# Kernel tuning notes

Measured on AMD Instinct MI355X. Metric: run time of the kernel, lower is better.

## Reference

```python
import jax, jax.numpy as jnp
import numpy as np

B, S, D = 2, 2048, 512
H, HD = 8, 64  # num_heads, hidden_dim; H*HD == D
FF = 2048
EPS = 1e-5


def layer_norm(x, gamma, beta):
    mu = jnp.mean(x, axis=-1, keepdims=True)
    var = jnp.mean(jnp.square(x - mu), axis=-1, keepdims=True)
    return (x - mu) * jax.lax.rsqrt(var + EPS) * gamma + beta


def setup_inputs() -> dict:
    key = jax.random.key(0)
    ks = jax.random.split(key, 16)
    s = 0.02
    return {
        "Q": jax.random.normal(ks[0], (B, S, D), jnp.float32),
        "K": jax.random.normal(ks[1], (B, S, D), jnp.float32),
        "V": jax.random.normal(ks[2], (B, S, D), jnp.float32),
        "mask": jax.random.randint(ks[3], (B, S, S), 0, 2, jnp.int32),
        "Wq": jax.random.normal(ks[4], (D, H * HD), jnp.float32) * s,
        "Wk": jax.random.normal(ks[5], (D, H * HD), jnp.float32) * s,
        "Wv": jax.random.normal(ks[6], (D, H * HD), jnp.float32) * s,
        "Wo": jax.random.normal(ks[7], (H * HD, D), jnp.float32) * s,
        "bo": jnp.zeros((D,), jnp.float32),
        "gamma": jnp.ones((D,), jnp.float32),
        "beta": jnp.zeros((D,), jnp.float32),
        "W1": jax.random.normal(ks[8], (D, FF), jnp.float32) * s,
        "b1": jnp.zeros((FF,), jnp.float32),
        "W2": jax.random.normal(ks[9], (FF, D), jnp.float32) * s,
        "b2": jnp.zeros((D,), jnp.float32),
    }


def reference(Q, K, V, mask, Wq, Wk, Wv, Wo, bo, gamma, beta, W1, b1, W2, b2):
    # NOTE: original torch code calls Z.masked_fill(...) non-inplace and drops
    # the result, so `mask` has no effect on the math. Sequence=False.
    X = V
    # Faithful (interleaving) reshape: [B, S, H*HD] -> [B*H, S, HD]
    q = (Q @ Wq).reshape(B * H, -1, HD)
    k = (K @ Wk).reshape(B * H, -1, HD)
    v = (V @ Wv).reshape(B * H, -1, HD)
    scale = jnp.sqrt(jnp.float32(D))  # sqrt(input_size[2]), not sqrt(hidden_dim)
    scores = jnp.einsum('bqd,bkd->bqk', q, k) / scale  # [B*H, S, S]
    attn = jax.nn.softmax(scores, axis=2)
    Z = jnp.einsum('bqk,bkd->bqd', attn, v)            # [B*H, S, HD]
    Z = Z.reshape(B, -1, H * HD) @ Wo + bo             # [B, S, D]
    Z = layer_norm(X + Z, gamma, beta)
    ffn = (Z @ W1 + b1) @ W2 + b2                      # no activation in source
    return layer_norm(Z + ffn, gamma, beta)
```

## Files before the change

kernel.cpp:

```cpp
#include <hip/hip_runtime.h>
#include <hip/hip_bf16.h>


typedef __hip_bfloat16 bf16;
typedef short s16x8 __attribute__((ext_vector_type(8)));
typedef short s16x4 __attribute__((ext_vector_type(4)));
typedef float f32x4 __attribute__((ext_vector_type(4)));

#if __has_builtin(__builtin_amdgcn_exp2f)
#define EXP2F(x) __builtin_amdgcn_exp2f(x)
#else
#define EXP2F(x) exp2f(x)
#endif

__device__ __forceinline__ int dtypeF32(const void* gamma) {
    return *(const unsigned int*)gamma == 0x3F800000u;
}
__device__ __forceinline__ float inElem(const void* p, size_t i, int f32) {
    return f32 ? ((const float*)p)[i]
               : __bfloat162float(((const bf16*)p)[i]);
}
__device__ __forceinline__ void outElem(void* p, size_t i, float v, int f32) {
    if (f32) ((float*)p)[i] = v;
    else     ((bf16*)p)[i] = __float2bfloat16(v);
}
__device__ __forceinline__ s16x8 load8bf(const void* p, size_t i, int f32) {
    if (f32) {
        const float* s = (const float*)p + i;
        const float4 a = *(const float4*)s;
        const float4 b = *(const float4*)(s + 4);
        bf16 t[8] = {__float2bfloat16(a.x), __float2bfloat16(a.y),
                     __float2bfloat16(a.z), __float2bfloat16(a.w),
                     __float2bfloat16(b.x), __float2bfloat16(b.y),
                     __float2bfloat16(b.z), __float2bfloat16(b.w)};
        return *(const s16x8*)t;
    }
    return *(const s16x8*)((const bf16*)p + i);
}
__device__ __forceinline__ void load8f(const void* p, size_t i, int f32, float* o) {
    if (f32) {
        const float* s = (const float*)p + i;
        const float4 a = *(const float4*)s;
        const float4 b = *(const float4*)(s + 4);
        o[0] = a.x; o[1] = a.y; o[2] = a.z; o[3] = a.w;
        o[4] = b.x; o[5] = b.y; o[6] = b.z; o[7] = b.w;
    } else {
        const s16x8 v = *(const s16x8*)((const bf16*)p + i);
#pragma unroll
        for (int j = 0; j < 8; ++j) o[j] = __bfloat162float(((const bf16*)&v)[j]);
    }
}
__device__ __forceinline__ void store8(void* p, size_t i, const float* v, int f32) {
    if (f32) {
        float4 a = {v[0], v[1], v[2], v[3]};
        float4 b = {v[4], v[5], v[6], v[7]};
        *(float4*)((float*)p + i) = a;
        *(float4*)((float*)p + i + 4) = b;
    } else {
        bf16 t[8];
#pragma unroll
        for (int j = 0; j < 8; ++j) t[j] = __float2bfloat16(v[j]);
        *(s16x8*)((bf16*)p + i) = *(const s16x8*)t;
    }
}

__device__ __forceinline__ void gll16(const bf16* g, unsigned short* l) {
    __builtin_amdgcn_global_load_lds(
        (const __attribute__((address_space(1))) unsigned int*)(const void*)g,
        (__attribute__((address_space(3))) unsigned int*)(void*)l,
        16, 0, 0);
}

__device__ __forceinline__ size_t kfAddr(int row, int col) {
    const int g = row >> 8;
    const int j = ((row & 255) << 3) + (col >> 6);
    const int d = col & 63;
    return ((size_t)g << 17) + ((j >> 4) << 10) + ((d >> 5) << 9) +
           (((d & 31) >> 3) << 7) + ((j & 15) << 3) + (d & 7);
}
__device__ __forceinline__ size_t vfAddr(int row, int col) {
    const int g = row >> 8;
    const int j = ((row & 255) << 3) + (col >> 6);
    const int d = col & 63;
    return ((size_t)g << 17) + ((j >> 4) << 10) + ((d >> 4) << 8) +
           (((j >> 2) & 3) << 6) + ((d & 15) << 2) + (j & 3);
}

__global__ __launch_bounds__(256) void tr_kernel(const void* __restrict__ s0,
                                                 const void* __restrict__ s1,
                                                 const void* __restrict__ s2,
                                                 const void* __restrict__ s3,
                                                 const void* __restrict__ s4,
                                                 bf16* __restrict__ WT4,
                                                 bf16* __restrict__ W2T,
                                                 float scale0,
                                                 const void* __restrict__ gamma,
                                                 const void* __restrict__ bo,
                                                 float* __restrict__ bo_f) {
    const int z = blockIdx.z;
    if (z == 0 && blockIdx.y == 16 && blockIdx.x == 0) {
        const int f32 = dtypeF32(gamma);
        bo_f[threadIdx.x] = inElem(bo, threadIdx.x, f32);
        bo_f[threadIdx.x + 256] = inElem(bo, threadIdx.x + 256, f32);
        return;
    }
    if (z < 4 && blockIdx.y >= 16) return;
    const int f32 = dtypeF32(gamma);
    const void* src = z == 0 ? s0 : (z == 1 ? s1 : (z == 2 ? s2 : (z == 3 ? s3 : s4)));
    const int R = (z == 4) ? 2048 : 512;
    const int C = 512;
    bf16* d = (z == 4) ? W2T : WT4 + (size_t)z * 512 * 512;
    const float sc = (z == 0) ? scale0 : 1.f;
    __shared__ bf16 T[32][33];
    const int tx = threadIdx.x & 31, ty = threadIdx.x >> 5;
    const int c0 = blockIdx.x * 32, r0 = blockIdx.y * 32;
#pragma unroll
    for (int i = 0; i < 4; ++i)
        T[ty + 8 * i][tx] = __float2bfloat16(
            sc * inElem(src, (size_t)(r0 + ty + 8 * i) * C + c0 + tx, f32));
    __syncthreads();
#pragma unroll
    for (int i = 0; i < 4; ++i)
        d[(size_t)(c0 + ty + 8 * i) * R + r0 + tx] = T[tx][ty + 8 * i];
}

__global__ __launch_bounds__(256) void proj_kernel(
    const void* __restrict__ Q, const void* __restrict__ K,
    const void* __restrict__ V, const bf16* __restrict__ WT4,
    bf16* __restrict__ Qp, bf16* __restrict__ KFo, bf16* __restrict__ VFo,
    const bf16* __restrict__ W2T, const void* __restrict__ W1,
    float* __restrict__ Wc32, const void* __restrict__ gamma) {
    __shared__ __align__(16) unsigned short smem[20480];

    const int f32 = dtypeF32(gamma);
    const int tid = threadIdx.x;
    const int w = tid >> 6, lane = tid & 63, quad = lane >> 4, l16 = lane & 15;
    const int sr = tid >> 2, sc = (tid & 3) * 8;
    const int blk = blockIdx.x;

    if (blk < 384) {
        typedef unsigned short AsT[64][32];
        typedef unsigned short BsT[256][32];
        AsT* As = (AsT*)smem;
        BsT* Bs = (BsT*)(smem + 4096);

        const int z = blk >> 7, rem = blk & 127, by = rem >> 1, bx = rem & 1;
        const void* A = z == 0 ? Q : (z == 1 ? K : V);
        const bf16* Bt = WT4 + (size_t)z * 512 * 512;
        const int row0 = by * 64, col0 = bx * 256;

        f32x4 acc[4][4];
#pragma unroll
        for (int rb = 0; rb < 4; ++rb)
#pragma unroll
            for (int nb = 0; nb < 4; ++nb) acc[rb][nb] = (f32x4){0.f, 0.f, 0.f, 0.f};

        const size_t aBase = (size_t)(row0 + sr) * 512 + sc;
        const bf16* gB = Bt + (size_t)(col0 + sr) * 512 + sc;

        {
            const s16x8 a0 = load8bf(A, aBase, f32);
#pragma unroll
            for (int c = 0; c < 4; ++c)
                gll16(gB + (size_t)c * 64 * 512, &Bs[0][c * 64 + sr][sc]);
            *(s16x8*)&As[0][sr][sc] = a0;
        }
        __syncthreads();

        for (int t = 0; t < 16; ++t) {
            const int cur = t & 1, nxt = cur ^ 1;
            s16x8 aN;
            if (t < 15) {
                const int k = (t + 1) * 32;
                aN = load8bf(A, aBase + k, f32);
#pragma unroll
                for (int c = 0; c < 4; ++c)
                    gll16(gB + k + (size_t)c * 64 * 512, &Bs[nxt][c * 64 + sr][sc]);
            }

            s16x8 af[4];
#pragma unroll
            for (int rb = 0; rb < 4; ++rb)
                af[rb] = *(const s16x8*)&As[cur][rb * 16 + l16][quad * 8];
#pragma unroll
            for (int nb = 0; nb < 4; ++nb) {
                const s16x8 bf = *(const s16x8*)&Bs[cur][w * 64 + nb * 16 + l16][quad * 8];
#pragma unroll
                for (int rb = 0; rb < 4; ++rb)
                    acc[rb][nb] = __builtin_amdgcn_mfma_f32_16x16x32_bf16(
                        af[rb], bf, acc[rb][nb], 0, 0, 0);
            }

            if (t < 15) {
                *(s16x8*)&As[nxt][sr][sc] = aN;
                __syncthreads();
            }
        }

#pragma unroll
        for (int rb = 0; rb < 4; ++rb)
#pragma unroll
            for (int nb = 0; nb < 4; ++nb) {
                const int col = col0 + w * 64 + nb * 16 + l16;
#pragma unroll
                for (int r = 0; r < 4; ++r) {
                    const int row = row0 + rb * 16 + quad * 4 + r;
                    const bf16 v = __float2bfloat16(acc[rb][nb][r]);
                    if (z == 0)      Qp[(size_t)row * 512 + col] = v;
                    else if (z == 1) KFo[kfAddr(row, col)] = v;
                    else             VFo[vfAddr(row, col)] = v;
                }
            }
    } else {
        unsigned short (*As)[40] = (unsigned short (*)[40])smem;
        unsigned short (*Bs)[40] = (unsigned short (*)[40])(smem + 2560);

        const int idx = blk - 384;
        const int bx = idx & 3, by = (idx >> 2) & 7, bz = idx >> 5;
        const int N = 512, Kd = 2048, kSlice = 512;
        const int wr = w >> 1, wc = w & 1;
        const int row0 = by * 64, col0 = bx * 128;
        const int kOff = bz * kSlice;
        float* C = Wc32 + (size_t)bz * N * N;

        f32x4 acc[2][4];
#pragma unroll
        for (int rb = 0; rb < 2; ++rb)
#pragma unroll
            for (int nb = 0; nb < 4; ++nb) acc[rb][nb] = (f32x4){0.f, 0.f, 0.f, 0.f};

        for (int k0 = kOff; k0 < kOff + kSlice; k0 += 32) {
            __syncthreads();
            *(s16x8*)&As[sr][sc] = *(const s16x8*)(W2T + (size_t)(row0 + sr) * Kd + k0 + sc);
            *(s16x8*)&Bs[sr][sc] = load8bf(W1, (size_t)(col0 + sr) * Kd + k0 + sc, f32);
            *(s16x8*)&Bs[sr + 64][sc] = load8bf(W1, (size_t)(col0 + sr + 64) * Kd + k0 + sc, f32);
            __syncthreads();

            s16x8 aF[2], bFr[4];
#pragma unroll
            for (int rb = 0; rb < 2; ++rb)
                aF[rb] = *(const s16x8*)&As[wr * 32 + rb * 16 + l16][quad * 8];
#pragma unroll
            for (int nb = 0; nb < 4; ++nb)
                bFr[nb] = *(const s16x8*)&Bs[wc * 64 + nb * 16 + l16][quad * 8];
#pragma unroll
            for (int rb = 0; rb < 2; ++rb)
#pragma unroll
                for (int nb = 0; nb < 4; ++nb)
                    acc[rb][nb] = __builtin_amdgcn_mfma_f32_16x16x32_bf16(
                        aF[rb], bFr[nb], acc[rb][nb], 0, 0, 0);
        }

#pragma unroll
        for (int rb = 0; rb < 2; ++rb)
#pragma unroll
            for (int nb = 0; nb < 4; ++nb) {
                const int col = col0 + wc * 64 + nb * 16 + l16;
#pragma unroll
                for (int r = 0; r < 4; ++r) {
                    const int row = row0 + wr * 32 + rb * 16 + quad * 4 + r;
                    C[(size_t)row * N + col] = acc[rb][nb][r];
                }
            }
    }
}

__global__ __launch_bounds__(512) void attn_mfma_kernel(const bf16* __restrict__ Qp,
                                                        const bf16* __restrict__ KF,
                                                        const bf16* __restrict__ VF,
                                                        bf16* __restrict__ Z) {
    __shared__ __align__(16) unsigned short KsF[2][2][8192];
    __shared__ __align__(16) unsigned short VsF[2][2][8192];

    const int tid = threadIdx.x;
    const int w = tid >> 6;
    const int lane = tid & 63;
    const int quad = lane >> 4;
    const int l16 = lane & 15;
    const int hg = w >> 2;
    const int wl = w & 3;
    const int sg = tid >> 8;
    const int stid = tid & 255;

    const int g = blockIdx.x & 15;
    const int qt = blockIdx.x >> 4;
    const int qbase = g * 2048 + qt * 128 + wl * 32 + l16;

    s16x8 bQ[2][2];
#pragma unroll
    for (int qf = 0; qf < 2; ++qf)
#pragma unroll
        for (int ks = 0; ks < 2; ++ks)
            bQ[qf][ks] = *(const s16x8*)(Qp + (size_t)(qbase + qf * 16) * 64 + ks * 32 + quad * 8);

    f32x4 o[2][4];
    f32x4 oSum[2];
#pragma unroll
    for (int qf = 0; qf < 2; ++qf) {
        oSum[qf] = (f32x4){0.f, 0.f, 0.f, 0.f};
#pragma unroll
        for (int db = 0; db < 4; ++db) o[qf][db] = (f32x4){0.f, 0.f, 0.f, 0.f};
    }
    const s16x4 aOnes = {(short)0x3F80, (short)0x3F80, (short)0x3F80, (short)0x3F80};

    const bf16* KFg = KF + (size_t)g * 131072;
    const bf16* VFg = VF + (size_t)g * 131072;
    const int tb = sg * 8;

#pragma unroll
    for (int c = 0; c < 4; ++c) {
        const int idx = c * 256 + stid;
        gll16(KFg + (size_t)tb * 8192 + idx * 8, &KsF[sg][0][idx * 8]);
        gll16(VFg + (size_t)tb * 8192 + idx * 8, &VsF[sg][0][idx * 8]);
    }
    __syncthreads();

    for (int t = 0; t < 8; ++t) {
        const int cur = t & 1, nxt = cur ^ 1;
        if (t < 7) {
            const bf16* kt = KFg + (size_t)(tb + t + 1) * 8192;
            const bf16* vt = VFg + (size_t)(tb + t + 1) * 8192;
#pragma unroll
            for (int c = 0; c < 4; ++c) {
                const int idx = c * 256 + stid;
                gll16(kt + (size_t)idx * 8, &KsF[sg][nxt][idx * 8]);
                gll16(vt + (size_t)idx * 8, &VsF[sg][nxt][idx * 8]);
            }
        }

#pragma unroll
        for (int h = 0; h < 2; ++h) {
            const unsigned short* Kh = &KsF[hg][cur][h * 4096];
            const unsigned short* Vh = &VsF[hg][cur][h * 4096];

            f32x4 st[2][4];
#pragma unroll
            for (int qf = 0; qf < 2; ++qf)
#pragma unroll
                for (int kb = 0; kb < 4; ++kb) st[qf][kb] = (f32x4){0.f, 0.f, 0.f, 0.f};
#pragma unroll
            for (int kb = 0; kb < 4; ++kb)
#pragma unroll
                for (int ks = 0; ks < 2; ++ks) {
                    const s16x8 aK = *(const s16x8*)&Kh[((kb * 2 + ks) * 64 + lane) * 8];
                    st[0][kb] = __builtin_amdgcn_mfma_f32_16x16x32_bf16(aK, bQ[0][ks], st[0][kb], 0, 0, 0);
                    st[1][kb] = __builtin_amdgcn_mfma_f32_16x16x32_bf16(aK, bQ[1][ks], st[1][kb], 0, 0, 0);
                }

            s16x4 bP[2][4];
#pragma unroll
            for (int qf = 0; qf < 2; ++qf)
#pragma unroll
                for (int kb = 0; kb < 4; ++kb) {
                    const float p0 = EXP2F(st[qf][kb][0]);
                    const float p1 = EXP2F(st[qf][kb][1]);
                    const float p2 = EXP2F(st[qf][kb][2]);
                    const float p3 = EXP2F(st[qf][kb][3]);
                    const unsigned lo = __builtin_amdgcn_perm(
                        __builtin_bit_cast(unsigned, p1), __builtin_bit_cast(unsigned, p0), 0x07060302u);
                    const unsigned hi = __builtin_amdgcn_perm(
                        __builtin_bit_cast(unsigned, p3), __builtin_bit_cast(unsigned, p2), 0x07060302u);
                    union { unsigned u[2]; s16x4 v; } cvt;
                    cvt.u[0] = lo; cvt.u[1] = hi;
                    bP[qf][kb] = cvt.v;
                }

#pragma unroll
            for (int kb = 0; kb < 4; ++kb) {
                oSum[0] = __builtin_amdgcn_mfma_f32_16x16x16bf16_1k(aOnes, bP[0][kb], oSum[0], 0, 0, 0);
                oSum[1] = __builtin_amdgcn_mfma_f32_16x16x16bf16_1k(aOnes, bP[1][kb], oSum[1], 0, 0, 0);
#pragma unroll
                for (int db = 0; db < 4; ++db) {
                    const s16x4 aV = *(const s16x4*)&Vh[((kb * 4 + db) * 64 + lane) * 4];
                    o[0][db] = __builtin_amdgcn_mfma_f32_16x16x16bf16_1k(aV, bP[0][kb], o[0][db], 0, 0, 0);
                    o[1][db] = __builtin_amdgcn_mfma_f32_16x16x16bf16_1k(aV, bP[1][kb], o[1][db], 0, 0, 0);
                }
            }
        }

        if (t < 7) __syncthreads();
    }

    float* mrg = (float*)&KsF[0][0][0];
    __syncthreads();
    if (hg == 1) {
#pragma unroll
        for (int qf = 0; qf < 2; ++qf) {
#pragma unroll
            for (int db = 0; db < 4; ++db)
#pragma unroll
                for (int r = 0; r < 4; ++r)
                    mrg[((qf * 16 + db * 4 + r) << 8) + wl * 64 + lane] = o[qf][db][r];
            mrg[((32 + qf) << 8) + wl * 64 + lane] = oSum[qf][0];
        }
    }
    __syncthreads();
    if (hg == 0) {
#pragma unroll
        for (int qf = 0; qf < 2; ++qf) {
            const float sTot = oSum[qf][0] + mrg[((32 + qf) << 8) + wl * 64 + lane];
            const float inv = 1.f / sTot;
            const size_t qrow = (size_t)(qbase + qf * 16);
#pragma unroll
            for (int db = 0; db < 4; ++db) {
                bf16 tmp[4];
#pragma unroll
                for (int r = 0; r < 4; ++r) {
                    const float vv = o[qf][db][r] +
                        mrg[((qf * 16 + db * 4 + r) << 8) + wl * 64 + lane];
                    tmp[r] = __float2bfloat16(vv * inv);
                }
                *(s16x4*)(Z + qrow * 64 + db * 16 + quad * 4) = *(const s16x4*)tmp;
            }
        }
    }
}

__global__ __launch_bounds__(256) void gemm_bt_kernel(
    const bf16* __restrict__ A, const bf16* __restrict__ Bt,
    const float* __restrict__ bias, bf16* __restrict__ C,
    int N, int K,
    const float* __restrict__ Cf, bf16* __restrict__ WcTo,
    const bf16* __restrict__ W2Tp, const void* __restrict__ b1,
    const void* __restrict__ b2, float* __restrict__ bcO,
    const void* __restrict__ gamma) {
    __shared__ __align__(16) unsigned short As[2][64][32];
    __shared__ __align__(16) unsigned short Bs[2][128][32];

    const int tid = threadIdx.x;
    if (blockIdx.x >= 4) {
        if (blockIdx.x < 8) {
            const int i = (((blockIdx.x - 4) * 64 + blockIdx.y) * 256 + tid) * 4;
            const int MN = 512 * 512;
            const float4 a = *(const float4*)(Cf + i);
            const float4 b4 = *(const float4*)(Cf + i + MN);
            const float4 c = *(const float4*)(Cf + i + 2 * MN);
            const float4 d = *(const float4*)(Cf + i + 3 * MN);
            bf16 t[4] = {__float2bfloat16(a.x + b4.x + c.x + d.x),
                         __float2bfloat16(a.y + b4.y + c.y + d.y),
                         __float2bfloat16(a.z + b4.z + c.z + d.z),
                         __float2bfloat16(a.w + b4.w + c.w + d.w)};
            *(s16x4*)(WcTo + i) = *(const s16x4*)t;
        } else {
            const int f32 = dtypeF32(gamma);
            const int w4 = tid >> 6, lane = tid & 63;
#pragma unroll
            for (int t = 0; t < 2; ++t) {
                const int n = blockIdx.y * 8 + w4 * 2 + t;
                const bf16* rowp = W2Tp + (size_t)n * 2048;
                float s = 0.f;
#pragma unroll
                for (int i = 0; i < 4; ++i) {
                    const int f = lane * 8 + 512 * i;
                    float b1v[8];
                    load8f(b1, f, f32, b1v);
                    const s16x8 r = *(const s16x8*)(rowp + f);
#pragma unroll
                    for (int j = 0; j < 8; ++j)
                        s += b1v[j] * __bfloat162float(((const bf16*)&r)[j]);
                }
#pragma unroll
                for (int off = 32; off; off >>= 1) s += __shfl_xor(s, off);
                if (lane == 0) bcO[n] = s + inElem(b2, n, f32);
            }
        }
        return;
    }

    const int w = tid >> 6, lane = tid & 63, quad = lane >> 4, l16 = lane & 15;
    const int wr = w >> 1, wc = w & 1;
    const int row0 = blockIdx.y * 64, col0 = blockIdx.x * 128;
    const int sr = tid >> 2, sc = (tid & 3) * 8;

    const bf16* gA  = A  + (size_t)(row0 + sr) * K + sc;
    const bf16* gB0 = Bt + (size_t)(col0 + sr) * K + sc;
    const bf16* gB1 = Bt + (size_t)(col0 + sr + 64) * K + sc;

    f32x4 acc[2][4];
#pragma unroll
    for (int rb = 0; rb < 2; ++rb)
#pragma unroll
        for (int nb = 0; nb < 4; ++nb) acc[rb][nb] = (f32x4){0.f, 0.f, 0.f, 0.f};

    const int nst = K >> 5;
    gll16(gA,  &As[0][sr][sc]);
    gll16(gB0, &Bs[0][sr][sc]);
    gll16(gB1, &Bs[0][sr + 64][sc]);
    __syncthreads();

    for (int t = 0; t < nst; ++t) {
        const int cur = t & 1, nxt = cur ^ 1;
        if (t + 1 < nst) {
            const int k = (t + 1) * 32;
            gll16(gA + k,  &As[nxt][sr][sc]);
            gll16(gB0 + k, &Bs[nxt][sr][sc]);
            gll16(gB1 + k, &Bs[nxt][sr + 64][sc]);
        }

        s16x8 aF[2], bF[4];
#pragma unroll
        for (int rb = 0; rb < 2; ++rb)
            aF[rb] = *(const s16x8*)&As[cur][wr * 32 + rb * 16 + l16][quad * 8];
#pragma unroll
        for (int nb = 0; nb < 4; ++nb)
            bF[nb] = *(const s16x8*)&Bs[cur][wc * 64 + nb * 16 + l16][quad * 8];
#pragma unroll
        for (int rb = 0; rb < 2; ++rb)
#pragma unroll
            for (int nb = 0; nb < 4; ++nb)
                acc[rb][nb] = __builtin_amdgcn_mfma_f32_16x16x32_bf16(
                    aF[rb], bF[nb], acc[rb][nb], 0, 0, 0);

        if (t + 1 < nst) __syncthreads();
    }

#pragma unroll
    for (int rb = 0; rb < 2; ++rb)
#pragma unroll
        for (int nb = 0; nb < 4; ++nb) {
            const int col = col0 + wc * 64 + nb * 16 + l16;
            const float bv = bias[col];
#pragma unroll
            for (int r = 0; r < 4; ++r) {
                const int row = row0 + wr * 32 + rb * 16 + quad * 4 + r;
                C[(size_t)row * N + col] = __float2bfloat16(acc[rb][nb][r] + bv);
            }
        }
}

__global__ __launch_bounds__(256) void ln_res_kernel(const void* __restrict__ X, int xMode,
                                                     const bf16* __restrict__ Zin,
                                                     const void* __restrict__ gamma,
                                                     const void* __restrict__ beta,
                                                     void* __restrict__ out, int oMode) {
    const int f = dtypeF32(gamma);
    const int xF = xMode == 2 ? f : xMode;
    const int oF = oMode == 2 ? f : oMode;
    const int row = blockIdx.x * 4 + (threadIdx.x >> 6);
    const int lane = threadIdx.x & 63;
    const size_t rb = (size_t)row * 512;
    const int c0 = lane * 8;

    float v[8];
    load8f(X, rb + c0, xF, v);
    const s16x8 z = *(const s16x8*)(Zin + rb + c0);
    float sum = 0.f, sumsq = 0.f;
#pragma unroll
    for (int i = 0; i < 8; ++i) {
        v[i] += __bfloat162float(((const bf16*)&z)[i]);
        sum += v[i];
        sumsq += v[i] * v[i];
    }
#pragma unroll
    for (int off = 32; off; off >>= 1) {
        sum += __shfl_xor(sum, off);
        sumsq += __shfl_xor(sumsq, off);
    }
    const float mu = sum * (1.f / 512.f);
    const float var = sumsq * (1.f / 512.f) - mu * mu;
    const float rs = rsqrtf(var + 1e-5f);
    float g[8], bt[8], o[8];
    load8f(gamma, c0, f, g);
    load8f(beta, c0, f, bt);
#pragma unroll
    for (int i = 0; i < 8; ++i) o[i] = (v[i] - mu) * rs * g[i] + bt[i];
    store8(out, rb + c0, o, oF);
}

extern "C" void kernel_launch(void* const* d_in, const int* in_sizes, int n_in,
                              void* d_out, int out_size, void* d_ws, size_t ws_size,
                              hipStream_t stream) {
    const void* Q     = d_in[0];
    const void* K     = d_in[1];
    const void* V     = d_in[2];
    const void* Wq    = d_in[4];
    const void* Wk    = d_in[5];
    const void* Wv    = d_in[6];
    const void* Wo    = d_in[7];
    const void* bo    = d_in[8];
    const void* gamma = d_in[9];
    const void* beta  = d_in[10];
    const void* W1    = d_in[11];
    const void* b1    = d_in[12];
    const void* W2    = d_in[13];
    const void* b2    = d_in[14];

    const size_t NT  = (size_t)4096 * 512;
    const size_t WSQ = 512 * 512;
    const size_t W1N = 512 * 2048;

    const size_t NEED = 26000000;
    char* scratch = (ws_size >= NEED) ? (char*)d_ws : (char*)d_in[3];

    bf16* base = (bf16*)scratch;
    bf16* Qp  = base;
    bf16* KF  = Qp + NT;
    bf16* VF  = KF + NT;
    bf16* Zt  = VF + NT;
    bf16* WT4 = Zt + NT;
    bf16* W2T = WT4 + 4 * WSQ;
    bf16* WcT = W2T + W1N;
    float* Wc32 = (float*)(WcT + WSQ);
    float* bc   = Wc32 + 4 * WSQ;
    float* bo_f = bc + 512;
    bf16* Zo = VF;
    bf16* Z1 = KF;
    bf16* Fo = (bf16*)Wc32;

    const dim3 blk(256);
    const float qscale = 1.4426950408889634f * 0.044194173824159216f;

    tr_kernel<<<dim3(16, 64, 5), blk, 0, stream>>>(Wq, Wk, Wv, Wo, W2,
                                                   WT4, W2T, qscale, gamma, bo, bo_f);

    proj_kernel<<<dim3(512), blk, 0, stream>>>(Q, K, V, WT4, Qp, KF, VF,
                                               W2T, W1, Wc32, gamma);

    attn_mfma_kernel<<<dim3(256), dim3(512), 0, stream>>>(Qp, KF, VF, Zt);

    gemm_bt_kernel<<<dim3(9, 64), blk, 0, stream>>>(Zt, WT4 + 3 * WSQ, bo_f, Zo,
                                                    512, 512,
                                                    Wc32, WcT, W2T, b1, b2, bc, gamma);

    ln_res_kernel<<<dim3(1024), blk, 0, stream>>>(V, 2, Zo, gamma, beta, Z1, 0);

    gemm_bt_kernel<<<dim3(4, 64), blk, 0, stream>>>(Z1, WcT, bc, Fo,
                                                    512, 512,
                                                    nullptr, nullptr, nullptr,
                                                    nullptr, nullptr, nullptr, gamma);

    ln_res_kernel<<<dim3(1024), blk, 0, stream>>>(Z1, 0, Fo, gamma, beta, d_out, 2);
}
```

Measured before the change: 199.6 us.

## Double K-tile depth in projection GEMMs and stage epilogue through LDS for vector stores

The QKV projection and the bias GEMM now load 64-wide K tiles per stage instead of 32, which halves the number of barriers and pipeline iterations. The projection epilogue now writes accumulators into a padded, XOR-swizzled LDS tile and then emits 16-byte vector stores into the Q, K-fragment and V-fragment layouts, replacing scattered 2-byte stores computed through kfAddr/vfAddr. In exchange, LDS use per block roughly doubles, which may lower occupancy, and the layout index math becomes more intricate.

```diff
diff --git a/kernel.cpp b/kernel.cpp
--- a/kernel.cpp
+++ b/kernel.cpp
@@ -69,21 +69,6 @@
         (const __attribute__((address_space(1))) unsigned int*)(const void*)g,
         (__attribute__((address_space(3))) unsigned int*)(void*)l,
         16, 0, 0);
-}
-
-__device__ __forceinline__ size_t kfAddr(int row, int col) {
-    const int g = row >> 8;
-    const int j = ((row & 255) << 3) + (col >> 6);
-    const int d = col & 63;
-    return ((size_t)g << 17) + ((j >> 4) << 10) + ((d >> 5) << 9) +
-           (((d & 31) >> 3) << 7) + ((j & 15) << 3) + (d & 7);
-}
-__device__ __forceinline__ size_t vfAddr(int row, int col) {
-    const int g = row >> 8;
-    const int j = ((row & 255) << 3) + (col >> 6);
-    const int d = col & 63;
-    return ((size_t)g << 17) + ((j >> 4) << 10) + ((d >> 4) << 8) +
-           (((j >> 2) & 3) << 6) + ((d & 15) << 2) + (j & 3);
 }
 
 __global__ __launch_bounds__(256) void tr_kernel(const void* __restrict__ s0,
@@ -130,7 +115,7 @@
     bf16* __restrict__ Qp, bf16* __restrict__ KFo, bf16* __restrict__ VFo,
     const bf16* __restrict__ W2T, const void* __restrict__ W1,
     float* __restrict__ Wc32, const void* __restrict__ gamma) {
-    __shared__ __align__(16) unsigned short smem[20480];
+    __shared__ __align__(16) unsigned short smem[40960];
 
     const int f32 = dtypeF32(gamma);
     const int tid = threadIdx.x;
@@ -139,10 +124,8 @@
     const int blk = blockIdx.x;
 
     if (blk < 384) {
-        typedef unsigned short AsT[64][32];
-        typedef unsigned short BsT[256][32];
-        AsT* As = (AsT*)smem;
-        BsT* Bs = (BsT*)(smem + 4096);
+        unsigned short* AsF = smem;
+        unsigned short* BsF = smem + 8192;
 
         const int z = blk >> 7, rem = blk & 127, by = rem >> 1, bx = rem & 1;
         const void* A = z == 0 ? Q : (z == 1 ? K : V);
@@ -156,61 +139,121 @@
             for (int nb = 0; nb < 4; ++nb) acc[rb][nb] = (f32x4){0.f, 0.f, 0.f, 0.f};
 
         const size_t aBase = (size_t)(row0 + sr) * 512 + sc;
-        const bf16* gB = Bt + (size_t)(col0 + sr) * 512 + sc;
 
         {
             const s16x8 a0 = load8bf(A, aBase, f32);
-#pragma unroll
-            for (int c = 0; c < 4; ++c)
-                gll16(gB + (size_t)c * 64 * 512, &Bs[0][c * 64 + sr][sc]);
-            *(s16x8*)&As[0][sr][sc] = a0;
+            const s16x8 a1 = load8bf(A, aBase + 32, f32);
+#pragma unroll
+            for (int c = 0; c < 8; ++c) {
+                const int ch = c * 256 + tid;
+                gll16(Bt + (size_t)(col0 + (ch >> 3)) * 512 + (ch & 7) * 8,
+                      BsF + ch * 8);
+            }
+            *(s16x8*)(AsF + sr * 64 + sc) = a0;
+            *(s16x8*)(AsF + sr * 64 + sc + 32) = a1;
         }
         __syncthreads();
 
-        for (int t = 0; t < 16; ++t) {
+        for (int t = 0; t < 8; ++t) {
             const int cur = t & 1, nxt = cur ^ 1;
-            s16x8 aN;
-            if (t < 15) {
-                const int k = (t + 1) * 32;
-                aN = load8bf(A, aBase + k, f32);
-#pragma unroll
-                for (int c = 0; c < 4; ++c)
-                    gll16(gB + k + (size_t)c * 64 * 512, &Bs[nxt][c * 64 + sr][sc]);
-            }
-
-            s16x8 af[4];
-#pragma unroll
-            for (int rb = 0; rb < 4; ++rb)
-                af[rb] = *(const s16x8*)&As[cur][rb * 16 + l16][quad * 8];
+            s16x8 aN0, aN1;
+            if (t < 7) {
+                const int k = (t + 1) * 64;
+                aN0 = load8bf(A, aBase + k, f32);
+                aN1 = load8bf(A, aBase + k + 32, f32);
+#pragma unroll
+                for (int c = 0; c < 8; ++c) {
+                    const int ch = c * 256 + tid;
+                    gll16(Bt + (size_t)(col0 + (ch >> 3)) * 512 + k + (ch & 7) * 8,
+                          BsF + nxt * 16384 + ch * 8);
+                }
+            }
+
+#pragma unroll
+            for (int kk = 0; kk < 2; ++kk) {
+                s16x8 af[4];
+#pragma unroll
+                for (int rb = 0; rb < 4; ++rb)
+                    af[rb] = *(const s16x8*)(AsF + cur * 4096 +
+                                             (rb * 16 + l16) * 64 + kk * 32 + quad * 8);
+#pragma unroll
+                for (int nb = 0; nb < 4; ++nb) {
+                    const s16x8 bfv = *(const s16x8*)(BsF + cur * 16384 +
+                                                      (w * 64 + nb * 16 + l16) * 64 +
+                                                      kk * 32 + quad * 8);
+#pragma unroll
+                    for (int rb = 0; rb < 4; ++rb)
+                        acc[rb][nb] = __builtin_amdgcn_mfma_f32_16x16x32_bf16(
+                            af[rb], bfv, acc[rb][nb], 0, 0, 0);
+                }
+            }
+
+            if (t < 7) {
+                *(s16x8*)(AsF + nxt * 4096 + sr * 64 + sc) = aN0;
+                *(s16x8*)(AsF + nxt * 4096 + sr * 64 + sc + 32) = aN1;
+                __syncthreads();
+            }
+        }
+
+        bf16 (*Ts)[264] = (bf16 (*)[264])smem;
+        __syncthreads();
+#pragma unroll
+        for (int rb = 0; rb < 4; ++rb)
 #pragma unroll
             for (int nb = 0; nb < 4; ++nb) {
-                const s16x8 bf = *(const s16x8*)&Bs[cur][w * 64 + nb * 16 + l16][quad * 8];
-#pragma unroll
-                for (int rb = 0; rb < 4; ++rb)
-                    acc[rb][nb] = __builtin_amdgcn_mfma_f32_16x16x32_bf16(
-                        af[rb], bf, acc[rb][nb], 0, 0, 0);
-            }
-
-            if (t < 15) {
-                *(s16x8*)&As[nxt][sr][sc] = aN;
-                __syncthreads();
-            }
-        }
-
-#pragma unroll
-        for (int rb = 0; rb < 4; ++rb)
-#pragma unroll
-            for (int nb = 0; nb < 4; ++nb) {
-                const int col = col0 + w * 64 + nb * 16 + l16;
-#pragma unroll
-                for (int r = 0; r < 4; ++r) {
-                    const int row = row0 + rb * 16 + quad * 4 + r;
-                    const bf16 v = __float2bfloat16(acc[rb][nb][r]);
-                    if (z == 0)      Qp[(size_t)row * 512 + col] = v;
-                    else if (z == 1) KFo[kfAddr(row, col)] = v;
-                    else             VFo[vfAddr(row, col)] = v;
-                }
-            }
+                const int cS = (w * 64 + nb * 16 + l16) ^ ((w & 3) << 3);
+#pragma unroll
+                for (int r = 0; r < 4; ++r)
+                    Ts[rb * 16 + quad * 4 + r][cS] = __float2bfloat16(acc[rb][nb][r]);
+            }
+        __syncthreads();
+
+        const int gq = by >> 2, r0p = by & 3;
+        if (z == 0) {
+#pragma unroll
+            for (int i = 0; i < 8; ++i) {
+                const int ch = i * 256 + tid;
+                const int rr = ch >> 5, cq = ch & 31;
+                const int cS = (cq * 8) ^ (((cq >> 3) & 3) << 3);
+                *(s16x8*)(Qp + (size_t)(row0 + rr) * 512 + col0 + cq * 8) =
+                    *(const s16x8*)&Ts[rr][cS];
+            }
+        } else if (z == 1) {
+            const int hh = tid & 3, qd = (tid >> 2) & 3, ks = (tid >> 4) & 1;
+            const int jbLo = tid >> 5;
+#pragma unroll
+            for (int i = 0; i < 8; ++i) {
+                const int rr0 = i & 1, jb = (i >> 1) * 8 + jbLo;
+                const int rr = jb * 2 + rr0;
+                const int cS = (hh * 64 + ks * 32 + qd * 8) ^ (hh << 3);
+                const size_t dst = (size_t)gq * 131072 +
+                                   (size_t)(r0p * 32 + jb) * 1024 +
+                                   ks * 512 + qd * 128 +
+                                   (rr0 * 8 + bx * 4 + hh) * 8;
+                *(s16x8*)(KFo + dst) = *(const s16x8*)&Ts[rr][cS];
+            }
+        } else {
+            const int dlh = tid & 7, db = (tid >> 3) & 3, rrLo = tid >> 5;
+#pragma unroll
+            for (int i = 0; i < 8; ++i) {
+                const int rr = i * 8 + rrLo;
+                const int qd2 = (rr & 1) * 2 + bx;
+                const int dl0 = dlh * 2;
+                unsigned rv[4];
+#pragma unroll
+                for (int h2 = 0; h2 < 4; ++h2)
+                    rv[h2] = *(const unsigned*)&Ts[rr][(h2 * 64 + db * 16 + dl0) ^ (h2 << 3)];
+                unsigned ou[4];
+                ou[0] = __builtin_amdgcn_perm(rv[1], rv[0], 0x05040100u);
+                ou[1] = __builtin_amdgcn_perm(rv[3], rv[2], 0x05040100u);
+                ou[2] = __builtin_amdgcn_perm(rv[1], rv[0], 0x07060302u);
+                ou[3] = __builtin_amdgcn_perm(rv[3], rv[2], 0x07060302u);
+                const size_t dst = (size_t)gq * 131072 +
+                                   (size_t)(r0p * 32 + (rr >> 1)) * 1024 +
+                                   db * 256 + qd2 * 64 + dl0 * 4;
+                *(uint4*)(VFo + dst) = *(const uint4*)ou;
+            }
+        }
     } else {
         unsigned short (*As)[40] = (unsigned short (*)[40])smem;
         unsigned short (*Bs)[40] = (unsigned short (*)[40])(smem + 2560);
@@ -424,8 +467,8 @@
     const bf16* __restrict__ W2Tp, const void* __restrict__ b1,
     const void* __restrict__ b2, float* __restrict__ bcO,
     const void* __restrict__ gamma) {
-    __shared__ __align__(16) unsigned short As[2][64][32];
-    __shared__ __align__(16) unsigned short Bs[2][128][32];
+    __shared__ __align__(16) unsigned short As[2][64][64];
+    __shared__ __align__(16) unsigned short Bs[2][128][64];
 
     const int tid = threadIdx.x;
     if (blockIdx.x >= 4) {
@@ -470,11 +513,6 @@
     const int w = tid >> 6, lane = tid & 63, quad = lane >> 4, l16 = lane & 15;
     const int wr = w >> 1, wc = w & 1;
     const int row0 = blockIdx.y * 64, col0 = blockIdx.x * 128;
-    const int sr = tid >> 2, sc = (tid & 3) * 8;
-
-    const bf16* gA  = A  + (size_t)(row0 + sr) * K + sc;
-    const bf16* gB0 = Bt + (size_t)(col0 + sr) * K + sc;
-    const bf16* gB1 = Bt + (size_t)(col0 + sr + 64) * K + sc;
 
     f32x4 acc[2][4];
 #pragma unroll
@@ -482,34 +520,55 @@
 #pragma unroll
         for (int nb = 0; nb < 4; ++nb) acc[rb][nb] = (f32x4){0.f, 0.f, 0.f, 0.f};
 
-    const int nst = K >> 5;
-    gll16(gA,  &As[0][sr][sc]);
-    gll16(gB0, &Bs[0][sr][sc]);
-    gll16(gB1, &Bs[0][sr + 64][sc]);
+    const int nst = K >> 6;
+#pragma unroll
+    for (int c = 0; c < 2; ++c) {
+        const int ch = c * 256 + tid;
+        gll16(A + (size_t)(row0 + (ch >> 3)) * K + (ch & 7) * 8,
+              &As[0][ch >> 3][(ch & 7) * 8]);
+    }
+#pragma unroll
+    for (int c = 0; c < 4; ++c) {
+        const int ch = c * 256 + tid;
+        gll16(Bt + (size_t)(col0 + (ch >> 3)) * K + (ch & 7) * 8,
+              &Bs[0][ch >> 3][(ch & 7) * 8]);
+    }
     __syncthreads();
 
     for (int t = 0; t < nst; ++t) {
         const int cur = t & 1, nxt = cur ^ 1;
         if (t + 1 < nst) {
-            const int k = (t + 1) * 32;
-            gll16(gA + k,  &As[nxt][sr][sc]);
-            gll16(gB0 + k, &Bs[nxt][sr][sc]);
-            gll16(gB1 + k, &Bs[nxt][sr + 64][sc]);
-        }
-
-        s16x8 aF[2], bF[4];
-#pragma unroll
-        for (int rb = 0; rb < 2; ++rb)
-            aF[rb] = *(const s16x8*)&As[cur][wr * 32 + rb * 16 + l16][quad * 8];
-#pragma unroll
-        for (int nb = 0; nb < 4; ++nb)
-            bF[nb] = *(const s16x8*)&Bs[cur][wc * 64 + nb * 16 + l16][quad * 8];
-#pragma unroll
-        for (int rb = 0; rb < 2; ++rb)
+            const int k = (t + 1) * 64;
+#pragma unroll
+            for (int c = 0; c < 2; ++c) {
+                const int ch = c * 256 + tid;
+                gll16(A + (size_t)(row0 + (ch >> 3)) * K + k + (ch & 7) * 8,
+                      &As[nxt][ch >> 3][(ch & 7) * 8]);
+            }
+#pragma unroll
+            for (int c = 0; c < 4; ++c) {
+                const int ch = c * 256 + tid;
+                gll16(Bt + (size_t)(col0 + (ch >> 3)) * K + k + (ch & 7) * 8,
+                      &Bs[nxt][ch >> 3][(ch & 7) * 8]);
+            }
+        }
+
+#pragma unroll
+        for (int kk = 0; kk < 2; ++kk) {
+            s16x8 aF[2], bF[4];
+#pragma unroll
+            for (int rb = 0; rb < 2; ++rb)
+                aF[rb] = *(const s16x8*)&As[cur][wr * 32 + rb * 16 + l16][kk * 32 + quad * 8];
 #pragma unroll
             for (int nb = 0; nb < 4; ++nb)
-                acc[rb][nb] = __builtin_amdgcn_mfma_f32_16x16x32_bf16(
-                    aF[rb], bF[nb], acc[rb][nb], 0, 0, 0);
+                bF[nb] = *(const s16x8*)&Bs[cur][wc * 64 + nb * 16 + l16][kk * 32 + quad * 8];
+#pragma unroll
+            for (int rb = 0; rb < 2; ++rb)
+#pragma unroll
+                for (int nb = 0; nb < 4; ++nb)
+                    acc[rb][nb] = __builtin_amdgcn_mfma_f32_16x16x32_bf16(
+                        aF[rb], bF[nb], acc[rb][nb], 0, 0, 0);
+        }
 
         if (t + 1 < nst) __syncthreads();
     }
```

Result: slower. 209.0 us (+4.7%).

## Halve attention LDS staging and split K/V prefetch to raise occupancy

Applied to the files above, without the earlier changes.

The attention kernel's shared-memory buffers shrink from 128KB to 64KB by staging 64-key units instead of 128-key tiles. K and V prefetches are now issued at separate points, each after a barrier, and a min-blocks hint of 4 is added to launch bounds. The aim is to fit more blocks per CU and hide the global-load latency better. The cost is twice as many loop iterations and more barriers per iteration, plus register pressure from the occupancy hint. The variable rename in the GEMM kernel is cosmetic.

```diff
diff --git a/kernel.cpp b/kernel.cpp
--- a/kernel.cpp
+++ b/kernel.cpp
@@ -184,11 +184,11 @@
                 af[rb] = *(const s16x8*)&As[cur][rb * 16 + l16][quad * 8];
 #pragma unroll
             for (int nb = 0; nb < 4; ++nb) {
-                const s16x8 bf = *(const s16x8*)&Bs[cur][w * 64 + nb * 16 + l16][quad * 8];
+                const s16x8 bfv = *(const s16x8*)&Bs[cur][w * 64 + nb * 16 + l16][quad * 8];
 #pragma unroll
                 for (int rb = 0; rb < 4; ++rb)
                     acc[rb][nb] = __builtin_amdgcn_mfma_f32_16x16x32_bf16(
-                        af[rb], bf, acc[rb][nb], 0, 0, 0);
+                        af[rb], bfv, acc[rb][nb], 0, 0, 0);
             }
 
             if (t < 15) {
@@ -265,12 +265,13 @@
     }
 }
 
-__global__ __launch_bounds__(512) void attn_mfma_kernel(const bf16* __restrict__ Qp,
-                                                        const bf16* __restrict__ KF,
-                                                        const bf16* __restrict__ VF,
-                                                        bf16* __restrict__ Z) {
-    __shared__ __align__(16) unsigned short KsF[2][2][8192];
-    __shared__ __align__(16) unsigned short VsF[2][2][8192];
+__global__ __launch_bounds__(512, 4) void attn_mfma_kernel(const bf16* __restrict__ Qp,
+                                                           const bf16* __restrict__ KF,
+                                                           const bf16* __restrict__ VF,
+                                                           bf16* __restrict__ Z) {
+    __shared__ __align__(16) unsigned short smem[32768];
+    unsigned short* Ks = smem;
+    unsigned short* Vs = smem + 16384;
 
     const int tid = threadIdx.x;
     const int w = tid >> 6;
@@ -305,83 +306,88 @@
 
     const bf16* KFg = KF + (size_t)g * 131072;
     const bf16* VFg = VF + (size_t)g * 131072;
-    const int tb = sg * 8;
-
-#pragma unroll
-    for (int c = 0; c < 4; ++c) {
+    const int su0 = sg * 16;
+
+#pragma unroll
+    for (int c = 0; c < 2; ++c) {
         const int idx = c * 256 + stid;
-        gll16(KFg + (size_t)tb * 8192 + idx * 8, &KsF[sg][0][idx * 8]);
-        gll16(VFg + (size_t)tb * 8192 + idx * 8, &VsF[sg][0][idx * 8]);
+        gll16(KFg + (size_t)su0 * 4096 + idx * 8, Ks + sg * 8192 + idx * 8);
+        gll16(VFg + (size_t)su0 * 4096 + idx * 8, Vs + sg * 8192 + idx * 8);
     }
     __syncthreads();
 
-    for (int t = 0; t < 8; ++t) {
-        const int cur = t & 1, nxt = cur ^ 1;
-        if (t < 7) {
-            const bf16* kt = KFg + (size_t)(tb + t + 1) * 8192;
-            const bf16* vt = VFg + (size_t)(tb + t + 1) * 8192;
-#pragma unroll
-            for (int c = 0; c < 4; ++c) {
+    for (int u = 0; u < 16; ++u) {
+        const int cur = u & 1, nxt = cur ^ 1;
+        const unsigned short* Kh = Ks + hg * 8192 + cur * 4096;
+        const unsigned short* Vh = Vs + hg * 8192 + cur * 4096;
+
+        f32x4 st[2][4];
+#pragma unroll
+        for (int kb = 0; kb < 4; ++kb) {
+            st[0][kb] = (f32x4){0.f, 0.f, 0.f, 0.f};
+            st[1][kb] = (f32x4){0.f, 0.f, 0.f, 0.f};
+        }
+#pragma unroll
+        for (int kb = 0; kb < 4; ++kb)
+#pragma unroll
+            for (int ks = 0; ks < 2; ++ks) {
+                const s16x8 aK = *(const s16x8*)&Kh[((kb * 2 + ks) * 64 + lane) * 8];
+                st[0][kb] = __builtin_amdgcn_mfma_f32_16x16x32_bf16(aK, bQ[0][ks], st[0][kb], 0, 0, 0);
+                st[1][kb] = __builtin_amdgcn_mfma_f32_16x16x32_bf16(aK, bQ[1][ks], st[1][kb], 0, 0, 0);
+            }
+
+        __syncthreads();
+        if (u < 15) {
+#pragma unroll
+            for (int c = 0; c < 2; ++c) {
                 const int idx = c * 256 + stid;
-                gll16(kt + (size_t)idx * 8, &KsF[sg][nxt][idx * 8]);
-                gll16(vt + (size_t)idx * 8, &VsF[sg][nxt][idx * 8]);
-            }
-        }
-
-#pragma unroll
-        for (int h = 0; h < 2; ++h) {
-            const unsigned short* Kh = &KsF[hg][cur][h * 4096];
-            const unsigned short* Vh = &VsF[hg][cur][h * 4096];
-
-            f32x4 st[2][4];
-#pragma unroll
-            for (int qf = 0; qf < 2; ++qf)
-#pragma unroll
-                for (int kb = 0; kb < 4; ++kb) st[qf][kb] = (f32x4){0.f, 0.f, 0.f, 0.f};
-#pragma unroll
-            for (int kb = 0; kb < 4; ++kb)
-#pragma unroll
-                for (int ks = 0; ks < 2; ++ks) {
-                    const s16x8 aK = *(const s16x8*)&Kh[((kb * 2 + ks) * 64 + lane) * 8];
-                    st[0][kb] = __builtin_amdgcn_mfma_f32_16x16x32_bf16(aK, bQ[0][ks], st[0][kb], 0, 0, 0);
-                    st[1][kb] = __builtin_amdgcn_mfma_f32_16x16x32_bf16(aK, bQ[1][ks], st[1][kb], 0, 0, 0);
-                }
-
-            s16x4 bP[2][4];
-#pragma unroll
-            for (int qf = 0; qf < 2; ++qf)
-#pragma unroll
-                for (int kb = 0; kb < 4; ++kb) {
-                    const float p0 = EXP2F(st[qf][kb][0]);
-                    const float p1 = EXP2F(st[qf][kb][1]);
-                    const float p2 = EXP2F(st[qf][kb][2]);
-                    const float p3 = EXP2F(st[qf][kb][3]);
-                    const unsigned lo = __builtin_amdgcn_perm(
-                        __builtin_bit_cast(unsigned, p1), __builtin_bit_cast(unsigned, p0), 0x07060302u);
-                    const unsigned hi = __builtin_amdgcn_perm(
-                        __builtin_bit_cast(unsigned, p3), __builtin_bit_cast(unsigned, p2), 0x07060302u);
-                    union { unsigned u[2]; s16x4 v; } cvt;
-                    cvt.u[0] = lo; cvt.u[1] = hi;
-                    bP[qf][kb] = cvt.v;
-                }
-
+                gll16(KFg + (size_t)(su0 + u + 1) * 4096 + idx * 8,
+                      Ks + sg * 8192 + nxt * 4096 + idx * 8);
+            }
+        }
+
+        s16x4 bP[2][4];
+#pragma unroll
+        for (int qf = 0; qf < 2; ++qf)
 #pragma unroll
             for (int kb = 0; kb < 4; ++kb) {
-                oSum[0] = __builtin_amdgcn_mfma_f32_16x16x16bf16_1k(aOnes, bP[0][kb], oSum[0], 0, 0, 0);
-                oSum[1] = __builtin_amdgcn_mfma_f32_16x16x16bf16_1k(aOnes, bP[1][kb], oSum[1], 0, 0, 0);
-#pragma unroll
-                for (int db = 0; db < 4; ++db) {
-                    const s16x4 aV = *(const s16x4*)&Vh[((kb * 4 + db) * 64 + lane) * 4];
-                    o[0][db] = __builtin_amdgcn_mfma_f32_16x16x16bf16_1k(aV, bP[0][kb], o[0][db], 0, 0, 0);
-                    o[1][db] = __builtin_amdgcn_mfma_f32_16x16x16bf16_1k(aV, bP[1][kb], o[1][db], 0, 0, 0);
-                }
-            }
-        }
-
-        if (t < 7) __syncthreads();
-    }
-
-    float* mrg = (float*)&KsF[0][0][0];
+                const float p0 = EXP2F(st[qf][kb][0]);
+                const float p1 = EXP2F(st[qf][kb][1]);
+                const float p2 = EXP2F(st[qf][kb][2]);
+                const float p3 = EXP2F(st[qf][kb][3]);
+                const unsigned lo = __builtin_amdgcn_perm(
+                    __builtin_bit_cast(unsigned, p1), __builtin_bit_cast(unsigned, p0), 0x07060302u);
+                const unsigned hi = __builtin_amdgcn_perm(
+                    __builtin_bit_cast(unsigned, p3), __builtin_bit_cast(unsigned, p2), 0x07060302u);
+                union { unsigned u2[2]; s16x4 v; } cvt;
+                cvt.u2[0] = lo; cvt.u2[1] = hi;
+                bP[qf][kb] = cvt.v;
+            }
+
+#pragma unroll
+        for (int kb = 0; kb < 4; ++kb) {
+            oSum[0] = __builtin_amdgcn_mfma_f32_16x16x16bf16_1k(aOnes, bP[0][kb], oSum[0], 0, 0, 0);
+            oSum[1] = __builtin_amdgcn_mfma_f32_16x16x16bf16_1k(aOnes, bP[1][kb], oSum[1], 0, 0, 0);
+#pragma unroll
+            for (int db = 0; db < 4; ++db) {
+                const s16x4 aV = *(const s16x4*)&Vh[((kb * 4 + db) * 64 + lane) * 4];
+                o[0][db] = __builtin_amdgcn_mfma_f32_16x16x16bf16_1k(aV, bP[0][kb], o[0][db], 0, 0, 0);
+                o[1][db] = __builtin_amdgcn_mfma_f32_16x16x16bf16_1k(aV, bP[1][kb], o[1][db], 0, 0, 0);
+            }
+        }
+
+        if (u < 15) {
+            __syncthreads();
+#pragma unroll
+            for (int c = 0; c < 2; ++c) {
+                const int idx = c * 256 + stid;
+                gll16(VFg + (size_t)(su0 + u + 1) * 4096 + idx * 8,
+                      Vs + sg * 8192 + nxt * 4096 + idx * 8);
+            }
+        }
+    }
+
+    float* mrg = (float*)smem;
     __syncthreads();
     if (hg == 1) {
 #pragma unroll
```

Measured after the change: 203.7 us. +2.0%, slower.
